# Performance work log

Hardware: AMD Instinct MI355X
Metric: run time of the kernel (lower is better)

Reference implementation:

```python
import jax, jax.numpy as jnp
import numpy as np

MAX_RADIUS = 4.0
N_BASIS = 10
MUL = 8                    # output_size -> '8x0e' multiplicity
OUT_MULS = (16, 8, 4)      # irreps_output = 16x0e + 8x1o + 4x2e
L_DIMS = (1, 3, 5)
N_NODES = 10000
N_EDGES = 131072
N_GRAPHS = 64
WEIGHT_NUMEL = MUL * MUL * sum(OUT_MULS)  # 1792


def _silu(x):
    return x * jax.nn.sigmoid(x)


def _sph_harm(u):
    # e3nn real spherical harmonics lmax=2, normalize=True, 'component' normalization
    x, y, z = u[:, 0], u[:, 1], u[:, 2]
    s3, s5, s15 = 3.0 ** 0.5, 5.0 ** 0.5, 15.0 ** 0.5
    sh0 = jnp.ones_like(x)[:, None]
    sh1 = jnp.stack([s3 * x, s3 * y, s3 * z], -1)
    sh2 = jnp.stack([s15 * x * z, s15 * x * y,
                     s5 * (y * y - 0.5 * (x * x + z * z)),
                     s15 * y * z, 0.5 * s15 * (z * z - x * x)], -1)
    return sh0, sh1, sh2


def _soft_one_hot(x):
    # e3nn soft_one_hot_linspace, basis='gaussian', cutoff=True
    values = jnp.linspace(0.0, MAX_RADIUS, N_BASIS + 2)[1:-1]
    step = MAX_RADIUS / (N_BASIS + 1)
    diff = (x[:, None] - values) / step
    return jnp.exp(-diff * diff) / 1.12


def setup_inputs() -> dict:
    key = jax.random.key(0)
    ks = jax.random.split(key, 16)
    return {
        "pos": jax.random.normal(ks[0], (N_NODES, 3), jnp.float32) * 2.0,
        "A": jax.random.randint(ks[1], (N_NODES,), 0, 10),
        "batch": jnp.sort(jax.random.randint(ks[2], (N_NODES,), 0, N_GRAPHS)),
        "edge_src": jax.random.randint(ks[3], (N_EDGES,), 0, N_NODES),
        "edge_dst": jax.random.randint(ks[4], (N_EDGES,), 0, N_NODES),
        "edge_shifts": jax.random.normal(ks[5], (N_EDGES, 3), jnp.float32) * 0.1,
        "cell": jax.random.normal(ks[6], (N_GRAPHS, 3, 3), jnp.float32),
        "embed_table": jax.random.normal(ks[7], (10, 16), jnp.float32),
        "fit_W1": jax.random.normal(ks[8], (16, 64), jnp.float32) * (2.0 / 16) ** 0.5,
        "fit_b1": jnp.zeros((64,), jnp.float32),
        "fit_W2": jax.random.normal(ks[9], (64, 32), jnp.float32) * (2.0 / 64) ** 0.5,
        "fit_b2": jnp.zeros((32,), jnp.float32),
        "fit_W3": jax.random.normal(ks[10], (32, MUL), jnp.float32) * (2.0 / 32) ** 0.5,
        "fit_b3": jnp.zeros((MUL,), jnp.float32),
        "fc_W1": jax.random.normal(ks[11], (N_BASIS, 64), jnp.float32),
        "fc_W2": jax.random.normal(ks[12], (64, 64), jnp.float32),
        "fc_W3": jax.random.normal(ks[13], (64, 64), jnp.float32),
        "fc_W4": jax.random.normal(ks[14], (64, WEIGHT_NUMEL), jnp.float32),
    }


def reference(pos, A, batch, edge_src, edge_dst, edge_shifts, cell,
              embed_table, fit_W1, fit_b1, fit_W2, fit_b2, fit_W3, fit_b3,
              fc_W1, fc_W2, fc_W3, fc_W4):
    # --- edge vectors with periodic shifts ---
    shift_vecs = jnp.einsum('ni,nij->nj', edge_shifts, cell[batch[edge_src]])
    edge_vec = pos[edge_dst] - pos[edge_src] + shift_vecs      # [E,3]
    edge_length = jnp.linalg.norm(edge_vec, axis=1)            # [E]
    unit = edge_vec / jnp.maximum(edge_length, 1e-9)[:, None]

    # --- per-node scalar features: embedding -> MLP (MainNet2) ---
    h = embed_table[A]
    h = _silu(h @ fit_W1 + fit_b1)
    h = _silu(h @ fit_W2 + fit_b2)
    Ai = h @ fit_W3 + fit_b3                                   # [N,8]

    sh0, sh1, sh2 = _sph_harm(unit)                            # [E,1],[E,3],[E,5]

    # --- radial MLP (e3nn FullyConnectedNet: silu, 1/sqrt(fan_in) weight scaling) ---
    emb = _soft_one_hot(edge_length) * (N_BASIS ** 0.5)
    w = _silu(emb @ fc_W1 / N_BASIS ** 0.5)
    w = _silu(w @ fc_W2 / 8.0)
    w = _silu(w @ fc_W3 / 8.0)
    w = w @ fc_W4 / 8.0                                        # [E,1792]

    Ai_src = Ai[edge_src]                                      # [E,8]
    Ai_dst = Ai[edge_dst]                                      # [E,8]

    # FullTensorProduct(8x0e, sh) is the outer product f_in[e,u,m] = Ai_src[e,u]*sh_l[e,m];
    # FullyConnectedTensorProduct with scalar irreps_in2 reduces per l-channel to a
    # weighted contraction with path normalization 1/sqrt(mul1*mul2) = 1/8.
    blocks, off = [], 0
    for mul_out, dim, sh_l in zip(OUT_MULS, L_DIMS, (sh0, sh1, sh2)):
        n = MUL * MUL * mul_out
        Wl = w[:, off:off + n].reshape(-1, MUL, MUL, mul_out)
        off += n
        blk = jnp.einsum('eu,em,ev,euvw->ewm', Ai_src, sh_l, Ai_dst, Wl) / MUL
        blocks.append(blk.reshape(-1, mul_out * dim))
    edge_features = jnp.concatenate(blocks, -1)                # [E,60]

    # --- scatter-mean aggregation to destination nodes ---
    n_nodes = pos.shape[0]
    counts = jax.ops.segment_sum(jnp.ones((edge_dst.shape[0],), jnp.float32),
                                 edge_dst, num_segments=n_nodes)
    out = jax.ops.segment_sum(edge_features, edge_dst, num_segments=n_nodes)
    return out / jnp.maximum(counts, 1.0)[:, None]             # [N,60]
```

## Files before the change

### kernel.cpp

```cpp
#include <hip/hip_runtime.h>
#include <hip/hip_bf16.h>
#include <math.h>

#define NN 10000
#define NE 131072

typedef __attribute__((ext_vector_type(8))) short short8;
typedef __attribute__((ext_vector_type(4))) float f32x4;

__device__ __forceinline__ float silu_f(float x) {
    return x / (1.0f + __expf(-x));
}

__device__ __forceinline__ unsigned short f2bf(float f) {
    unsigned int u = __float_as_uint(f);
    u += 0x7FFFu + ((u >> 16) & 1u);
    return (unsigned short)(u >> 16);
}

__device__ __forceinline__ unsigned int pk_bf16(float lo, float hi) {
    __hip_bfloat162 h = __float22bfloat162_rn(float2{lo, hi});
    return *reinterpret_cast<unsigned int*>(&h);
}

__global__ __launch_bounds__(256)
void prep_kernel(const int* __restrict__ A,
                 const int* __restrict__ edst,
                 const float* __restrict__ emb_tab,
                 const float* __restrict__ W1, const float* __restrict__ b1,
                 const float* __restrict__ W2, const float* __restrict__ b2,
                 const float* __restrict__ W3, const float* __restrict__ b3,
                 const float* __restrict__ fcW1,
                 const float* __restrict__ fcW2,
                 const float* __restrict__ fcW3,
                 const float* __restrict__ fcW4,
                 int* __restrict__ hist,
                 int* __restrict__ rank,
                 float* __restrict__ outg,
                 float* __restrict__ Ai,
                 unsigned short* __restrict__ Wg,
                 unsigned short* __restrict__ Bg)
{
    const int blk = blockIdx.x;
    const int tid = threadIdx.x;

    if (blk < 40) {
        int nd = blk * 256 + tid;
        if (nd >= NN) return;
        int a = A[nd];
        float h[16];
#pragma unroll
        for (int i = 0; i < 16; ++i) h[i] = emb_tab[a * 16 + i];
        float h1[64];
#pragma unroll
        for (int j = 0; j < 64; ++j) h1[j] = b1[j];
#pragma unroll
        for (int i = 0; i < 16; ++i) {
            float hv = h[i];
#pragma unroll
            for (int j = 0; j < 64; ++j) h1[j] += hv * W1[i * 64 + j];
        }
#pragma unroll
        for (int j = 0; j < 64; ++j) h1[j] = silu_f(h1[j]);
        float h2[32];
#pragma unroll
        for (int j = 0; j < 32; ++j) h2[j] = b2[j];
#pragma unroll
        for (int i = 0; i < 64; ++i) {
            float hv = h1[i];
#pragma unroll
            for (int j = 0; j < 32; ++j) h2[j] += hv * W2[i * 32 + j];
        }
#pragma unroll
        for (int j = 0; j < 32; ++j) h2[j] = silu_f(h2[j]);
#pragma unroll
        for (int j = 0; j < 8; ++j) {
            float s = b3[j];
#pragma unroll
            for (int i = 0; i < 32; ++i) s += h2[i] * W3[i * 8 + j];
            Ai[nd * 8 + j] = s;
        }
    } else if (blk < 80) {
        int i = (blk - 40) * 256 + tid;
        int j    = i & 7;
        int lane = (i >> 3) & 63;
        int f    = i >> 9;
        int q = lane >> 4, n = lane & 15;
        int L, kf, nt;
        if (f < 4)       { L = 1; kf = 0;             nt = f; }
        else if (f < 12) { L = 2; kf = (f - 4) >> 2;  nt = (f - 4) & 3; }
        else             { L = 3; kf = (f - 12) >> 2; nt = (f - 12) & 3; }
        int k = kf * 32 + q * 8 + j;
        int col = nt * 16 + n;
        float v = 0.0f;
        if (L == 1)      { if (k < 10) v = fcW1[k * 64 + col]; }
        else if (L == 2) v = fcW2[k * 64 + col];
        else             v = fcW3[k * 64 + col];
        Wg[i] = f2bf(v);
    } else if (blk < 592) {
        int linear = (blk - 80) * 256 + tid;
        rank[linear] = atomicAdd(&hist[edst[linear]], 1);
        if (linear < 114688) {
            int k = linear / 1792;
            int t = linear - k * 1792;
            int uv, wc;
            if (t < 1024)      { uv = t >> 4;            wc = t & 15; }
            else if (t < 1536) { int r = t - 1024; uv = r >> 3; wc = 16 + (r & 7); }
            else               { int r = t - 1536; uv = r >> 2; wc = 24 + (r & 3); }
            int h  = uv >> 5;
            int q  = (uv >> 3) & 3;
            int j  = uv & 7;
            int nt = wc >> 4;
            int n  = wc & 15;
            int i  = (k << 11) | (h << 10) | (nt << 9) | (((q << 4) | n) << 3) | j;
            Bg[i] = f2bf(fcW4[linear]);
        } else {
            int z  = linear - 114688;
            int k  = z >> 8;
            int r  = z & 255;
            int uv = r >> 2;
            int c2 = z & 3;
            int h  = uv >> 5;
            int q  = (uv >> 3) & 3;
            int j  = uv & 7;
            int i  = (k << 11) | (h << 10) | (1 << 9) | (((q << 4) | (12 + c2)) << 3) | j;
            Bg[i] = 0;
        }
    } else {
        int t = (blk - 592) * 256 + tid;
        float4 z = float4{0.f, 0.f, 0.f, 0.f};
        for (int r = t; r < 150000; r += 25600)
            ((float4*)outg)[r] = z;
    }
}

__global__ __launch_bounds__(256)
void scanrank_kernel(const int* __restrict__ edst,
                     const int* __restrict__ hist,
                     const int* __restrict__ rank,
                     int* __restrict__ sortidx)
{
    __shared__ int offs[NN];
    __shared__ int part[256];
    const int tid = threadIdx.x;

    int loc[40];
    int s = 0;
    if (tid < 250) {
        const int4* h4 = (const int4*)(hist) + tid * 10;
#pragma unroll
        for (int v = 0; v < 10; ++v) {
            int4 x = h4[v];
            loc[v * 4 + 0] = x.x; loc[v * 4 + 1] = x.y;
            loc[v * 4 + 2] = x.z; loc[v * 4 + 3] = x.w;
            s += x.x + x.y + x.z + x.w;
        }
    } else {
#pragma unroll
        for (int r = 0; r < 40; ++r) loc[r] = 0;
    }
    part[tid] = s;
    __syncthreads();
#pragma unroll
    for (int off = 1; off < 256; off <<= 1) {
        int v = (tid >= off) ? part[tid - off] : 0;
        __syncthreads();
        part[tid] += v;
        __syncthreads();
    }
    if (tid < 250) {
        int run = part[tid] - s;
        int base = tid * 40;
#pragma unroll
        for (int r = 0; r < 40; ++r) { offs[base + r] = run; run += loc[r]; }
    }
    __syncthreads();

    int e = blockIdx.x * 256 + tid;
    int d = edst[e];
    sortidx[offs[d] + rank[e]] = e;
}

__global__ __launch_bounds__(256, 2)
void edge_fused_kernel(const float* __restrict__ pos,
                       const int* __restrict__ batch,
                       const int* __restrict__ esrc,
                       const int* __restrict__ edst,
                       const float* __restrict__ shifts,
                       const float* __restrict__ cell,
                       const unsigned short* __restrict__ Wg,
                       const unsigned short* __restrict__ Bg,
                       const int* __restrict__ sortidx,
                       const float* __restrict__ Ai,
                       const int* __restrict__ hist,
                       float* __restrict__ out_g)
{
    __shared__ __align__(16) unsigned char  WBs[20480];
    __shared__ __align__(16) unsigned short actb[4][64 * 68];
    __shared__ int   sdb[256];
    __shared__ __align__(16) float shb[4][64 * 8];

    const int tid  = threadIdx.x;
    const int wave = tid >> 6;
    const int lane = tid & 63;
    const int q    = lane >> 4;
    const int n    = lane & 15;
    const int i    = blockIdx.x * 256 + wave * 64 + lane;

#pragma unroll
    for (int it = 0; it < 5; ++it) {
        int idx = it * 256 + tid;
        const unsigned short* gp = Wg + idx * 8;
        unsigned char* lb = WBs + (it * 256 + wave * 64) * 16;
        __builtin_amdgcn_global_load_lds(
            (const __attribute__((address_space(1))) unsigned int*)gp,
            (__attribute__((address_space(3))) unsigned int*)lb, 16, 0, 0);
    }

    unsigned short* actw = actb[wave];

    int e = sortidx[i];
    int s = esrc[e], d = edst[e];
    sdb[wave * 64 + lane] = s | (d << 16);
    int b = batch[s];
    const float* C = cell + b * 9;
    float sx = shifts[e * 3 + 0], sy = shifts[e * 3 + 1], sz = shifts[e * 3 + 2];
    float vx = pos[d * 3 + 0] - pos[s * 3 + 0] + sx * C[0] + sy * C[3] + sz * C[6];
    float vy = pos[d * 3 + 1] - pos[s * 3 + 1] + sx * C[1] + sy * C[4] + sz * C[7];
    float vz = pos[d * 3 + 2] - pos[s * 3 + 2] + sx * C[2] + sy * C[5] + sz * C[8];
    float len = sqrtf(vx * vx + vy * vy + vz * vz);
    float inv = 1.0f / fmaxf(len, 1e-9f);
    float ux = vx * inv, uy = vy * inv, uz = vz * inv;
    {
        const float s3c  = 1.7320508075688772f;
        const float s5c  = 2.2360679774997896f;
        const float s15c = 3.872983346207417f;
        float* shw = shb[wave];
        *(float4*)&shw[lane * 8]     = float4{s3c * ux, s3c * uy, s3c * uz,
                                              s15c * ux * uz};
        *(float4*)&shw[lane * 8 + 4] = float4{s15c * ux * uy,
                                              s5c * (uy * uy - 0.5f * (ux * ux + uz * uz)),
                                              s15c * uy * uz,
                                              0.5f * s15c * (uz * uz - ux * ux)};
    }

    float embv[10];
    float base = len * 2.75f;
#pragma unroll
    for (int ii = 0; ii < 10; ++ii) {
        float ddv = base - (float)(ii + 1);
        embv[ii] = __expf(-ddv * ddv) * (1.0f / 1.12f);
    }
    {
        unsigned int u0 = pk_bf16(embv[0], embv[1]);
        unsigned int u1 = pk_bf16(embv[2], embv[3]);
        unsigned int u2 = pk_bf16(embv[4], embv[5]);
        unsigned int u3 = pk_bf16(embv[6], embv[7]);
        unsigned int u4 = pk_bf16(embv[8], embv[9]);
        uint2* arow = (uint2*)&actw[lane * 68];
        arow[0] = uint2{u0, u1};
        arow[1] = uint2{u2, u3};
        arow[2] = uint2{u4, 0u};
        arow[3] = uint2{0u, 0u};
        arow[4] = uint2{0u, 0u};
        arow[5] = uint2{0u, 0u};
        arow[6] = uint2{0u, 0u};
        arow[7] = uint2{0u, 0u};
    }

    __syncthreads();

    union AF { unsigned int u[4]; short8 s8; };
    const f32x4 Z4 = (f32x4){0.f, 0.f, 0.f, 0.f};
    const unsigned short* Wbuf = (const unsigned short*)WBs;

    auto loadA = [&](int t, int kf) -> AF {
        const unsigned short* ap = &actw[(t * 16 + n) * 68 + kf * 32 + q * 8];
        uint2 a = *(const uint2*)ap;
        uint2 c = *(const uint2*)(ap + 4);
        AF f; f.u[0] = a.x; f.u[1] = a.y; f.u[2] = c.x; f.u[3] = c.y;
        return f;
    };
    auto loadW = [&](int f) -> short8 {
        return *(const short8*)&Wbuf[(f * 64 + lane) * 8];
    };

    {
        AF A1[4];
#pragma unroll
        for (int t = 0; t < 4; ++t) A1[t] = loadA(t, 0);
#pragma unroll
        for (int nt = 0; nt < 4; ++nt) {
            short8 W0 = loadW(nt);
            f32x4 Cc[4];
#pragma unroll
            for (int t = 0; t < 4; ++t)
                Cc[t] = __builtin_amdgcn_mfma_f32_16x16x32_bf16(A1[t].s8, W0, Z4, 0, 0, 0);
#pragma unroll
            for (int t = 0; t < 4; ++t)
#pragma unroll
                for (int r = 0; r < 4; ++r)
                    actw[(t * 16 + q * 4 + r) * 68 + nt * 16 + n] = f2bf(silu_f(Cc[t][r]));
        }
    }

    {
        AF A2[4][2];
#pragma unroll
        for (int t = 0; t < 4; ++t)
#pragma unroll
            for (int kf = 0; kf < 2; ++kf) A2[t][kf] = loadA(t, kf);
#pragma unroll
        for (int nt = 0; nt < 4; ++nt) {
            short8 Wk0 = loadW(4 + nt);
            short8 Wk1 = loadW(8 + nt);
            f32x4 Cc[4];
#pragma unroll
            for (int t = 0; t < 4; ++t) {
                Cc[t] = __builtin_amdgcn_mfma_f32_16x16x32_bf16(A2[t][0].s8, Wk0, Z4, 0, 0, 0);
                Cc[t] = __builtin_amdgcn_mfma_f32_16x16x32_bf16(A2[t][1].s8, Wk1, Cc[t], 0, 0, 0);
            }
#pragma unroll
            for (int t = 0; t < 4; ++t)
#pragma unroll
                for (int r = 0; r < 4; ++r)
                    actw[(t * 16 + q * 4 + r) * 68 + nt * 16 + n] = f2bf(silu_f(Cc[t][r] * 0.125f));
        }
    }

    {
        AF A3[4][2];
#pragma unroll
        for (int t = 0; t < 4; ++t)
#pragma unroll
            for (int kf = 0; kf < 2; ++kf) A3[t][kf] = loadA(t, kf);
#pragma unroll
        for (int nt = 0; nt < 4; ++nt) {
            short8 Wk0 = loadW(12 + nt);
            short8 Wk1 = loadW(16 + nt);
            f32x4 Cc[4];
#pragma unroll
            for (int t = 0; t < 4; ++t) {
                Cc[t] = __builtin_amdgcn_mfma_f32_16x16x32_bf16(A3[t][0].s8, Wk0, Z4, 0, 0, 0);
                Cc[t] = __builtin_amdgcn_mfma_f32_16x16x32_bf16(A3[t][1].s8, Wk1, Cc[t], 0, 0, 0);
            }
#pragma unroll
            for (int t = 0; t < 4; ++t)
#pragma unroll
                for (int r = 0; r < 4; ++r)
                    actw[(nt * 16 + n) * 68 + t * 16 + q * 4 + r] = f2bf(silu_f(Cc[t][r] * 0.125f));
        }
    }

    __syncthreads();

    auto stageB = [&](int c, int buf) {
#pragma unroll
        for (int it = 0; it < 2; ++it) {
            int idx = it * 256 + tid;
            const unsigned char* gp = ((const unsigned char*)Bg) + c * 8192 + idx * 16;
            unsigned char* lb = WBs + buf * 8192 + (it * 256 + wave * 64) * 16;
            __builtin_amdgcn_global_load_lds(
                (const __attribute__((address_space(1))) unsigned int*)gp,
                (__attribute__((address_space(3))) unsigned int*)lb, 16, 0, 0);
        }
    };
    stageB(0, 0);

    AF P[4][2];
#pragma unroll
    for (int t = 0; t < 4; ++t) {
        int eL = wave * 64 + t * 16 + n;
        int sd = sdb[eL];
        int ss  = sd & 0xFFFF;
        int dd2 = sd >> 16;
        float As0 = Ai[ss * 8 + q];
        float As1 = Ai[ss * 8 + 4 + q];
        float4 d0 = *(const float4*)&Ai[dd2 * 8];
        float4 d1 = *(const float4*)&Ai[dd2 * 8 + 4];
        float Ad[8] = {d0.x, d0.y, d0.z, d0.w, d1.x, d1.y, d1.z, d1.w};
#pragma unroll
        for (int h = 0; h < 2; ++h) {
            float s0 = h ? As1 : As0;
            P[t][h].u[0] = pk_bf16(s0 * Ad[0], s0 * Ad[1]);
            P[t][h].u[1] = pk_bf16(s0 * Ad[2], s0 * Ad[3]);
            P[t][h].u[2] = pk_bf16(s0 * Ad[4], s0 * Ad[5]);
            P[t][h].u[3] = pk_bf16(s0 * Ad[6], s0 * Ad[7]);
        }
    }

    f32x4 out[4][2];
#pragma unroll
    for (int t = 0; t < 4; ++t)
#pragma unroll
        for (int nt = 0; nt < 2; ++nt)
            out[t][nt] = (f32x4){0.f, 0.f, 0.f, 0.f};

    __syncthreads();

#pragma unroll 1
    for (int c = 0; c < 32; ++c) {
        int cur = c & 1;
        if (c < 31) stageB(c + 1, cur ^ 1);
#pragma unroll
        for (int kk = 0; kk < 2; ++kk) {
            int k = c * 2 + kk;
            short8 Bf[2][2];
#pragma unroll
            for (int h = 0; h < 2; ++h)
#pragma unroll
                for (int nt = 0; nt < 2; ++nt)
                    Bf[h][nt] = *(const short8*)(WBs + cur * 8192 +
                                 ((kk * 2 + h) * 2 + nt) * 1024 + lane * 16);
#pragma unroll
            for (int t = 0; t < 4; ++t) {
                uint2 v = *(const uint2*)&actw[k * 68 + t * 16 + q * 4];
                float w0 = __uint_as_float(v.x << 16);
                float w1 = __uint_as_float(v.x & 0xFFFF0000u);
                float w2 = __uint_as_float(v.y << 16);
                float w3 = __uint_as_float(v.y & 0xFFFF0000u);
#pragma unroll
                for (int nt = 0; nt < 2; ++nt) {
                    f32x4 Q = __builtin_amdgcn_mfma_f32_16x16x32_bf16(
                        P[t][0].s8, Bf[0][nt], Z4, 0, 0, 0);
                    Q = __builtin_amdgcn_mfma_f32_16x16x32_bf16(
                        P[t][1].s8, Bf[1][nt], Q, 0, 0, 0);
                    out[t][nt][0] += w0 * Q[0];
                    out[t][nt][1] += w1 * Q[1];
                    out[t][nt][2] += w2 * Q[2];
                    out[t][nt][3] += w3 * Q[3];
                }
            }
        }
        __syncthreads();
    }

    float* featL = (float*)actw;
#pragma unroll
    for (int t = 0; t < 4; ++t) {
#pragma unroll
        for (int r = 0; r < 4; ++r) {
            int row = t * 16 + q * 4 + r;
            featL[row * 33 + n]      = out[t][0][r];
            featL[row * 33 + 16 + n] = out[t][1][r];
        }
    }

    if (lane < 60) {
        int j = lane;
        int cc, sidx = 0;
        bool is0 = (j < 16);
        if (j < 16)      { cc = j; }
        else if (j < 40) { cc = 16 + (j - 16) / 3; sidx = (j - 16) % 3; }
        else             { cc = 24 + (j - 40) / 5; sidx = 3 + (j - 40) % 5; }

        const float* shw = shb[wave];
        int cur_d = sdb[wave * 64] >> 16;
        float acc = 0.f;
        for (int e2 = 0; e2 < 64; ++e2) {
            int d_e = sdb[wave * 64 + e2] >> 16;
            if (d_e != cur_d) {
                int cnt = hist[cur_d];
                atomicAdd(&out_g[cur_d * 60 + j], acc * (1.0f / 64.0f) / (float)cnt);
                acc = 0.f;
                cur_d = d_e;
            }
            float f  = featL[e2 * 33 + cc];
            float sh = shw[e2 * 8 + sidx];
            if (is0) sh = 1.0f;
            acc += f * sh;
        }
        int cnt = hist[cur_d];
        atomicAdd(&out_g[cur_d * 60 + j], acc * (1.0f / 64.0f) / (float)cnt);
    }
}

extern "C" void kernel_launch(void* const* d_in, const int* in_sizes, int n_in,
                              void* d_out, int out_size, void* d_ws, size_t ws_size,
                              hipStream_t stream)
{
    const float* pos     = (const float*)d_in[0];
    const int*   A       = (const int*)d_in[1];
    const int*   batch   = (const int*)d_in[2];
    const int*   esrc    = (const int*)d_in[3];
    const int*   edst    = (const int*)d_in[4];
    const float* shifts  = (const float*)d_in[5];
    const float* cell    = (const float*)d_in[6];
    const float* emb_tab = (const float*)d_in[7];
    const float* fitW1   = (const float*)d_in[8];
    const float* fitb1   = (const float*)d_in[9];
    const float* fitW2   = (const float*)d_in[10];
    const float* fitb2   = (const float*)d_in[11];
    const float* fitW3   = (const float*)d_in[12];
    const float* fitb3   = (const float*)d_in[13];
    const float* fcW1    = (const float*)d_in[14];
    const float* fcW2    = (const float*)d_in[15];
    const float* fcW3    = (const float*)d_in[16];
    const float* fcW4    = (const float*)d_in[17];

    float* out = (float*)d_out;

    char* W = (char*)d_ws;
    float* Ai      = (float*)W;  W += (size_t)NN * 8 * 4;
    int* sortidx   = (int*)W;    W += (size_t)NE * 4;
    int* rank      = (int*)W;    W += (size_t)NE * 4;
    int* hist      = (int*)W;    W += (size_t)NN * 4;
    unsigned short* Bg = (unsigned short*)W; W += (size_t)131072 * 2;
    unsigned short* Wg = (unsigned short*)W; W += (size_t)10240 * 2;

    hipMemsetAsync(hist, 0, (size_t)NN * 4, stream);

    prep_kernel<<<692, 256, 0, stream>>>(
        A, edst, emb_tab, fitW1, fitb1, fitW2, fitb2, fitW3, fitb3,
        fcW1, fcW2, fcW3, fcW4, hist, rank, out, Ai, Wg, Bg);

    scanrank_kernel<<<NE / 256, 256, 0, stream>>>(edst, hist, rank, sortidx);

    edge_fused_kernel<<<NE / 256, 256, 0, stream>>>(
        pos, batch, esrc, edst, shifts, cell, Wg, Bg,
        sortidx, Ai, hist, out);
}
```

Baseline: 192.3 us.

## Read MLP and tensor-product weights directly from global memory, drop LDS staging

Weight fragments for the radial MLP and the per-chunk tensor-product B matrix are now loaded straight from global memory (L1/L2 cached) into registers. This replaces the async global-to-LDS double-buffered staging. Dropping it removes the 20 KB shared buffer and the per-chunk __syncthreads barriers, which should allow more blocks per CU and less barrier stalling. The cost is that every wave issues its own global loads for the same shared weights, with L2/L1 latency exposed inside the MFMA loop, and the loop is unrolled by 2.

```diff
diff --git a/kernel.cpp b/kernel.cpp
--- a/kernel.cpp
+++ b/kernel.cpp
@@ -195,7 +195,6 @@
                        const int* __restrict__ hist,
                        float* __restrict__ out_g)
 {
-    __shared__ __align__(16) unsigned char  WBs[20480];
     __shared__ __align__(16) unsigned short actb[4][64 * 68];
     __shared__ int   sdb[256];
     __shared__ __align__(16) float shb[4][64 * 8];
@@ -206,16 +205,6 @@
     const int q    = lane >> 4;
     const int n    = lane & 15;
     const int i    = blockIdx.x * 256 + wave * 64 + lane;
-
-#pragma unroll
-    for (int it = 0; it < 5; ++it) {
-        int idx = it * 256 + tid;
-        const unsigned short* gp = Wg + idx * 8;
-        unsigned char* lb = WBs + (it * 256 + wave * 64) * 16;
-        __builtin_amdgcn_global_load_lds(
-            (const __attribute__((address_space(1))) unsigned int*)gp,
-            (__attribute__((address_space(3))) unsigned int*)lb, 16, 0, 0);
-    }
 
     unsigned short* actw = actb[wave];
 
@@ -268,11 +257,8 @@
         arow[7] = uint2{0u, 0u};
     }
 
-    __syncthreads();
-
     union AF { unsigned int u[4]; short8 s8; };
     const f32x4 Z4 = (f32x4){0.f, 0.f, 0.f, 0.f};
-    const unsigned short* Wbuf = (const unsigned short*)WBs;
 
     auto loadA = [&](int t, int kf) -> AF {
         const unsigned short* ap = &actw[(t * 16 + n) * 68 + kf * 32 + q * 8];
@@ -282,7 +268,7 @@
         return f;
     };
     auto loadW = [&](int f) -> short8 {
-        return *(const short8*)&Wbuf[(f * 64 + lane) * 8];
+        return *(const short8*)&Wg[(f * 64 + lane) * 8];
     };
 
     {
@@ -351,21 +337,6 @@
                     actw[(nt * 16 + n) * 68 + t * 16 + q * 4 + r] = f2bf(silu_f(Cc[t][r] * 0.125f));
         }
     }
-
-    __syncthreads();
-
-    auto stageB = [&](int c, int buf) {
-#pragma unroll
-        for (int it = 0; it < 2; ++it) {
-            int idx = it * 256 + tid;
-            const unsigned char* gp = ((const unsigned char*)Bg) + c * 8192 + idx * 16;
-            unsigned char* lb = WBs + buf * 8192 + (it * 256 + wave * 64) * 16;
-            __builtin_amdgcn_global_load_lds(
-                (const __attribute__((address_space(1))) unsigned int*)gp,
-                (__attribute__((address_space(3))) unsigned int*)lb, 16, 0, 0);
-        }
-    };
-    stageB(0, 0);
 
     AF P[4][2];
 #pragma unroll
@@ -396,12 +367,9 @@
         for (int nt = 0; nt < 2; ++nt)
             out[t][nt] = (f32x4){0.f, 0.f, 0.f, 0.f};
 
-    __syncthreads();
-
-#pragma unroll 1
+    const unsigned char* BgB = (const unsigned char*)Bg;
+#pragma unroll 2
     for (int c = 0; c < 32; ++c) {
-        int cur = c & 1;
-        if (c < 31) stageB(c + 1, cur ^ 1);
 #pragma unroll
         for (int kk = 0; kk < 2; ++kk) {
             int k = c * 2 + kk;
@@ -410,8 +378,8 @@
             for (int h = 0; h < 2; ++h)
 #pragma unroll
                 for (int nt = 0; nt < 2; ++nt)
-                    Bf[h][nt] = *(const short8*)(WBs + cur * 8192 +
-                                 ((kk * 2 + h) * 2 + nt) * 1024 + lane * 16);
+                    Bf[h][nt] = *(const short8*)(BgB +
+                        (((size_t)((c * 8 + kk * 4 + h * 2 + nt) * 64 + lane)) << 4));
 #pragma unroll
             for (int t = 0; t < 4; ++t) {
                 uint2 v = *(const uint2*)&actw[k * 68 + t * 16 + q * 4];
@@ -432,7 +400,6 @@
                 }
             }
         }
-        __syncthreads();
     }
 
     float* featL = (float*)actw;
```

After: 196.2 us. +2.0%, slower.
